# Performance work log

Hardware: AMD Instinct MI355X
Metric: run time of the kernel (lower is better)

Reference implementation:

```python
import jax, jax.numpy as jnp
import numpy as np

HEADS = 8
DIM_HEAD = 64
SCALE = DIM_HEAD ** (-0.5)


def setup_inputs() -> dict:
    key = jax.random.key(0)
    ks = jax.random.split(key, 6)
    x = jax.random.normal(ks[0], (4, 2048, 1024), dtype=jnp.float32)
    context = jax.random.normal(ks[1], (4, 512, 768), dtype=jnp.float32)
    # linear weights stored as (in, out); init scaled like nn.Linear default-ish
    Wq = jax.random.normal(ks[2], (1024, 512), dtype=jnp.float32) * (1.0 / np.sqrt(1024))
    Wk = jax.random.normal(ks[3], (768, 512), dtype=jnp.float32) * (1.0 / np.sqrt(768))
    Wv = jax.random.normal(ks[4], (768, 512), dtype=jnp.float32) * (1.0 / np.sqrt(768))
    Wo = jax.random.normal(ks[5], (512, 1024), dtype=jnp.float32) * (1.0 / np.sqrt(512))
    return {"x": x, "context": context, "Wq": Wq, "Wk": Wk, "Wv": Wv, "Wo": Wo}


def reference(x, context, Wq, Wk, Wv, Wo):
    # projections: [b, i, inner], [b, j, inner]
    q = jnp.einsum('bid,de->bie', x, Wq)
    k = jnp.einsum('bjd,de->bje', context, Wk)
    v = jnp.einsum('bjd,de->bje', context, Wv)
    b, i, _ = q.shape
    j = k.shape[1]
    # split heads: [b, h, seq, c]
    q = q.reshape(b, i, HEADS, DIM_HEAD).transpose(0, 2, 1, 3)
    k = k.reshape(b, j, HEADS, DIM_HEAD).transpose(0, 2, 1, 3)
    v = v.reshape(b, j, HEADS, DIM_HEAD).transpose(0, 2, 1, 3)
    scores = jnp.einsum('bhic,bhjc->bhij', q, k) * SCALE
    attn = jax.nn.softmax(scores, axis=-1)
    out = jnp.einsum('bhij,bhjc->bhic', attn, v)  # [b, h, i, c]
    out = out.transpose(0, 2, 1, 3).reshape(b, i, HEADS * DIM_HEAD)
    return jnp.einsum('bie,ed->bid', out, Wo)
```

## Files before the change

kernel.cpp:

```cpp
#include <hip/hip_runtime.h>
#include <stdint.h>

typedef unsigned short u16;
typedef __attribute__((ext_vector_type(8))) short short8;
typedef __attribute__((ext_vector_type(4))) float f32x4;

#define MFMA16(a, b, c) __builtin_amdgcn_mfma_f32_16x16x32_bf16((a), (b), (c), 0, 0, 0)

__device__ __forceinline__ u16 f2bf(float f) {
  unsigned int u = __float_as_uint(f);
  u += 0x7FFFu + ((u >> 16) & 1u);
  return (u16)(u >> 16);
}

__device__ __forceinline__ void gload16(const void* g, u16* lds) {
  __builtin_amdgcn_global_load_lds(
      (const __attribute__((address_space(1))) unsigned int*)g,
      (__attribute__((address_space(3))) unsigned int*)lds, 16, 0, 0);
}

__global__ void prep_all(const float* __restrict__ x, u16* __restrict__ xb, int n4x,
                         const float* __restrict__ cx, u16* __restrict__ cb, int n4c,
                         const float* __restrict__ Wq, const float* __restrict__ Wk,
                         const float* __restrict__ Wv, const float* __restrict__ Wo,
                         u16* __restrict__ wqT, u16* __restrict__ wkvT,
                         u16* __restrict__ woT) {
  __shared__ float tile[32][33];
  int z = blockIdx.z;
  int tx = threadIdx.x, ty = threadIdx.y;
  if (z == 4) {
    int bid = blockIdx.y * 32 + blockIdx.x;
    int tid = ty * 32 + tx;
    int idx = bid * 256 + tid, stride = 1024 * 256;
    int total = n4x + n4c;
    for (int i2 = idx; i2 < total; i2 += stride) {
      float4 v = (i2 < n4x) ? ((const float4*)x)[i2] : ((const float4*)cx)[i2 - n4x];
      ushort4 o;
      o.x = f2bf(v.x); o.y = f2bf(v.y); o.z = f2bf(v.z); o.w = f2bf(v.w);
      if (i2 < n4x) ((ushort4*)xb)[i2] = o; else ((ushort4*)cb)[i2 - n4x] = o;
    }
    return;
  }
  const float* src; u16* dst; int R, C; float scale = 1.0f;
  if (z == 0)      { src = Wq; dst = wqT;  R = 1024; C = 512;  scale = 0.125f; }
  else if (z == 1) { src = Wk; dst = wkvT; R = 768;  C = 512;  }
  else if (z == 2) { src = Wv; dst = wkvT + (size_t)512 * 768; R = 768; C = 512; }
  else             { src = Wo; dst = woT;  R = 512;  C = 1024; }
  int bx = blockIdx.x * 32, by = blockIdx.y * 32;
  if (bx >= C || by >= R) return;
#pragma unroll
  for (int i = 0; i < 4; ++i)
    tile[ty + 8 * i][tx] = src[(size_t)(by + ty + 8 * i) * C + bx + tx];
  __syncthreads();
#pragma unroll
  for (int i = 0; i < 4; ++i)
    dst[(size_t)(bx + ty + 8 * i) * R + by + tx] = f2bf(tile[tx][ty + 8 * i] * scale);
}

template <int MODE>
__device__ __forceinline__ void gemm_body(const u16* __restrict__ A,
                                          const u16* __restrict__ BT,
                                          void* __restrict__ C0p,
                                          void* __restrict__ C1p,
                                          int tm, int tn, int K, int N, u16* smem) {
  u16* As = smem;
  u16* Bs = smem + 8192;
  const int t = threadIdx.x;
  const int w = t >> 6, l = t & 63, lr = l & 15, lg = l >> 4;
  const int wr = w >> 1, wc = w & 1;

  f32x4 acc[4][2];
#pragma unroll
  for (int mi = 0; mi < 4; ++mi)
#pragma unroll
    for (int ni = 0; ni < 2; ++ni) acc[mi][ni] = (f32x4){0.f, 0.f, 0.f, 0.f};

  for (int kt = 0; kt < K; kt += 64) {
#pragma unroll
    for (int p = 0; p < 4; ++p) {
      int idx = p * 256 + t, row = idx >> 3, cg = idx & 7;
      gload16(A + (size_t)(tm + row) * K + kt + ((cg ^ (row & 7)) * 8),
              As + (p * 256 + (t & 192)) * 8);
    }
#pragma unroll
    for (int pb = 0; pb < 2; ++pb) {
      int idx = pb * 256 + t, row = idx >> 3, cg = idx & 7;
      gload16(BT + (size_t)(tn + row) * K + kt + ((cg ^ (row & 7)) * 8),
              Bs + (pb * 256 + (t & 192)) * 8);
    }
    __syncthreads();
    short8 af[4][2], bf[2][2];
#pragma unroll
    for (int mi = 0; mi < 4; ++mi)
#pragma unroll
      for (int kk = 0; kk < 2; ++kk)
        af[mi][kk] = *(const short8*)
            &As[(wr * 64 + mi * 16 + lr) * 64 + (((kk * 4 + lg) ^ (lr & 7)) * 8)];
#pragma unroll
    for (int ni = 0; ni < 2; ++ni)
#pragma unroll
      for (int kk = 0; kk < 2; ++kk)
        bf[ni][kk] = *(const short8*)
            &Bs[(wc * 32 + ni * 16 + lr) * 64 + (((kk * 4 + lg) ^ (lr & 7)) * 8)];
#pragma unroll
    for (int mi = 0; mi < 4; ++mi)
#pragma unroll
      for (int ni = 0; ni < 2; ++ni) {
        acc[mi][ni] = MFMA16(af[mi][0], bf[ni][0], acc[mi][ni]);
        acc[mi][ni] = MFMA16(af[mi][1], bf[ni][1], acc[mi][ni]);
      }
    __syncthreads();
  }

  if (MODE == 2 && tn >= 512) {
    u16* tile = smem;
#pragma unroll
    for (int mi = 0; mi < 4; ++mi)
#pragma unroll
      for (int ni = 0; ni < 2; ++ni) {
        ushort4 pk;
        pk.x = f2bf(acc[mi][ni][0]); pk.y = f2bf(acc[mi][ni][1]);
        pk.z = f2bf(acc[mi][ni][2]); pk.w = f2bf(acc[mi][ni][3]);
        *(ushort4*)&tile[(wc * 32 + ni * 16 + lr) * 136 + wr * 64 + mi * 16 + lg * 4] = pk;
      }
    __syncthreads();
    int bh = ((tm >> 9) << 3) + ((tn - 512) >> 6);
    u16* dst = (u16*)C1p + (size_t)bh * 64 * 512 + (tm & 511);
#pragma unroll
    for (int p = 0; p < 4; ++p) {
      int c = (p * 256 + t) >> 4, jj = (t & 15) * 8;
      short8 v = *(const short8*)&tile[c * 136 + jj];
      *(short8*)(dst + (size_t)c * 512 + jj) = v;
    }
    return;
  }

#pragma unroll
  for (int mi = 0; mi < 4; ++mi)
#pragma unroll
    for (int ni = 0; ni < 2; ++ni)
#pragma unroll
      for (int r = 0; r < 4; ++r) {
        int rg = tm + wr * 64 + mi * 16 + lg * 4 + r;
        int cg = tn + wc * 32 + ni * 16 + lr;
        float val = acc[mi][ni][r];
        if (MODE == 0) {
          ((float*)C0p)[(size_t)rg * N + cg] = val;
        } else if (MODE == 1) {
          ((u16*)C0p)[(((size_t)(rg >> 11) * 8 + (cg >> 6)) * 2048 + (rg & 2047)) * 64 +
                      (cg & 63)] = f2bf(val);
        } else {
          ((u16*)C0p)[(((size_t)(rg >> 9) * 8 + (cg >> 6)) * 512 + (rg & 511)) * 64 +
                      (cg & 63)] = f2bf(val);
        }
      }
}

__global__ __launch_bounds__(256) void gemm_qkv(const u16* __restrict__ xb,
                                                const u16* __restrict__ wqT,
                                                u16* __restrict__ qhb,
                                                const u16* __restrict__ cb,
                                                const u16* __restrict__ wkvT,
                                                u16* __restrict__ khb,
                                                u16* __restrict__ vtb) {
  __shared__ __align__(16) u16 smem[12288];
  int gid = (int)blockIdx.x;
  gid = (gid & 7) * 96 + (gid >> 3);
  if (gid < 512) {
    gemm_body<1>(xb, wqT, qhb, nullptr, (gid >> 3) * 128, (gid & 7) * 64, 1024, 512, smem);
  } else {
    int g2 = gid - 512;
    gemm_body<2>(cb, wkvT, khb, vtb, (g2 >> 4) * 128, (g2 & 15) * 64, 768, 1024, smem);
  }
}

__global__ __launch_bounds__(256) void gemm_o(const u16* __restrict__ aob,
                                              const u16* __restrict__ woT,
                                              float* __restrict__ out) {
  __shared__ __align__(16) u16 smem[12288];
  int gid = (int)blockIdx.x;
  gid = (gid & 7) * 128 + (gid >> 3);
  gemm_body<0>(aob, woT, out, nullptr, (gid >> 4) * 128, (gid & 15) * 64, 512, 1024, smem);
}

__global__ __launch_bounds__(512, 2) void attn_kernel(const u16* __restrict__ qhb,
                                                      const u16* __restrict__ khb,
                                                      const u16* __restrict__ vtb,
                                                      u16* __restrict__ aob) {
  __shared__ __align__(16) u16 kb[512 * 64];
  __shared__ __align__(16) u16 vb[64 * 512];
  __shared__ __align__(16) u16 pl[8][16 * 64];
  const int t = threadIdx.x, w = t >> 6, l = t & 63, i = l & 15, g = l >> 4;
  int lid = (int)blockIdx.x;
  lid = (lid & 7) * 64 + (lid >> 3);
  const int bh = lid >> 4, qh = lid & 15;
  const int i7 = i & 7;
  const int row0 = qh * 128 + w * 16;

  const u16* qp = qhb + ((size_t)bh * 2048 + row0) * 64;
  const u16* kp = khb + (size_t)bh * 512 * 64;
  const u16* vp = vtb + (size_t)bh * 64 * 512;

  short8 qa0 = *(const short8*)(qp + (size_t)i * 64 + g * 8);
  short8 qa1 = *(const short8*)(qp + (size_t)i * 64 + 32 + g * 8);

  const int wbase = (t & 448) * 8;

#pragma unroll
  for (int p = 0; p < 8; ++p) {
    int s = p * 512 + t;
    int r = s >> 3, cg = s & 7;
    gload16(kp + (size_t)r * 64 + ((cg ^ (r & 7)) * 8), kb + p * 4096 + wbase);
  }
#pragma unroll
  for (int p = 0; p < 8; ++p) {
    int s = p * 512 + t;
    int r = s >> 6, cg = s & 63;
    gload16(vp + (size_t)r * 512 + ((cg ^ (r & 7)) * 8), vb + p * 4096 + wbase);
  }
  __syncthreads();

  f32x4 sc[32];
#pragma unroll
  for (int jt = 0; jt < 32; ++jt) {
    int r = jt * 16 + i;
    short8 k0 = *(const short8*)&kb[r * 64 + ((g ^ i7) * 8)];
    short8 k1 = *(const short8*)&kb[r * 64 + (((4 + g) ^ i7) * 8)];
    f32x4 a = (f32x4){0.f, 0.f, 0.f, 0.f};
    a = MFMA16(k0, qa0, a);
    a = MFMA16(k1, qa1, a);
    sc[jt] = a;
  }

  f32x4 vm = sc[0];
#pragma unroll
  for (int jt = 1; jt < 32; ++jt) {
#pragma unroll
    for (int r = 0; r < 4; ++r) vm[r] = fmaxf(vm[r], sc[jt][r]);
  }
  float mx = fmaxf(fmaxf(vm[0], vm[1]), fmaxf(vm[2], vm[3]));
  mx = fmaxf(mx, __shfl_xor(mx, 16));
  mx = fmaxf(mx, __shfl_xor(mx, 32));
  float sum = 0.f;
#pragma unroll
  for (int jt = 0; jt < 32; ++jt) {
#pragma unroll
    for (int r = 0; r < 4; ++r) {
      float e = __expf(sc[jt][r] - mx);
      sc[jt][r] = e;
      sum += e;
    }
  }
  sum += __shfl_xor(sum, 16);
  sum += __shfl_xor(sum, 32);
  float inv = 1.f / sum;

  u16* pw = pl[w];
  f32x4 oac[4];
#pragma unroll
  for (int ct = 0; ct < 4; ++ct) oac[ct] = (f32x4){0.f, 0.f, 0.f, 0.f};

#pragma unroll
  for (int c8 = 0; c8 < 8; ++c8) {
#pragma unroll
    for (int tt = 0; tt < 4; ++tt) {
      int jt = c8 * 4 + tt;
      unsigned w0, w1;
      asm("v_cvt_pk_bf16_f32 %0, %1, %2" : "=v"(w0) : "v"(sc[jt][0]), "v"(sc[jt][1]));
      asm("v_cvt_pk_bf16_f32 %0, %1, %2" : "=v"(w1) : "v"(sc[jt][2]), "v"(sc[jt][3]));
      uint2 pk2; pk2.x = w0; pk2.y = w1;
      *(uint2*)&pw[i * 64 + ((tt * 16 + g * 4) ^ (i7 * 8))] = pk2;
    }
    asm volatile("s_waitcnt lgkmcnt(0)" ::: "memory");
    __builtin_amdgcn_sched_barrier(0);
#pragma unroll
    for (int T2 = 0; T2 < 2; ++T2) {
      short8 pa = *(const short8*)&pw[i * 64 + ((T2 * 32 + g * 8) ^ (i7 * 8))];
      int jg = c8 * 8 + T2 * 4 + g;
#pragma unroll
      for (int ct = 0; ct < 4; ++ct) {
        int vr = ct * 16 + i;
        short8 vf = *(const short8*)&vb[vr * 512 + ((jg ^ (vr & 7)) * 8)];
        oac[ct] = MFMA16(pa, vf, oac[ct]);
      }
    }
    asm volatile("" ::: "memory");
  }

  float iv[4];
#pragma unroll
  for (int r = 0; r < 4; ++r) iv[r] = __shfl(inv, (l & 48) + g * 4 + r);
  u16* op = aob + ((size_t)(bh >> 3) * 2048 + row0) * 512 + (bh & 7) * 64;
#pragma unroll
  for (int ct = 0; ct < 4; ++ct)
#pragma unroll
    for (int r = 0; r < 4; ++r)
      op[(size_t)(g * 4 + r) * 512 + ct * 16 + i] = f2bf(oac[ct][r] * iv[r]);
}

extern "C" void kernel_launch(void* const* d_in, const int* in_sizes, int n_in,
                              void* d_out, int out_size, void* d_ws, size_t ws_size,
                              hipStream_t stream) {
  const float* x  = (const float*)d_in[0];
  const float* cx = (const float*)d_in[1];
  const float* Wq = (const float*)d_in[2];
  const float* Wk = (const float*)d_in[3];
  const float* Wv = (const float*)d_in[4];
  const float* Wo = (const float*)d_in[5];
  float* out = (float*)d_out;

  char* p = (char*)d_ws;
  u16* xb   = (u16*)p; p += (size_t)8388608 * 2;
  u16* cb   = (u16*)p; p += (size_t)1572864 * 2;
  u16* wqT  = (u16*)p; p += (size_t)524288 * 2;
  u16* wkvT = (u16*)p; p += (size_t)786432 * 2;
  u16* woT  = (u16*)p; p += (size_t)524288 * 2;
  u16* qhb  = (u16*)p; p += (size_t)4194304 * 2;
  u16* khb  = (u16*)p; p += (size_t)1048576 * 2;
  u16* vtb  = (u16*)p; p += (size_t)1048576 * 2;
  u16* aob  = (u16*)p; p += (size_t)4194304 * 2;

  prep_all<<<dim3(32, 32, 5), dim3(32, 8), 0, stream>>>(
      x, xb, 8388608 / 4, cx, cb, 1572864 / 4, Wq, Wk, Wv, Wo, wqT, wkvT, woT);
  gemm_qkv<<<768, 256, 0, stream>>>(xb, wqT, qhb, cb, wkvT, khb, vtb);
  attn_kernel<<<512, 512, 0, stream>>>(qhb, khb, vtb, aob);
  gemm_o<<<1024, 256, 0, stream>>>(aob, woT, out);
}
```

Baseline: 67.59 us.

## Double-buffer LDS tiles in GEMM kernels to overlap global loads with MFMA

Splits the GEMM shared-memory staging into two buffers. The next K-tile is issued with global_load_lds while MFMAs run on the current tile, which hides global-load latency behind compute. LDS per block doubles to 48 KB, which may reduce occupancy. Only one barrier per iteration remains, and ordering depends on the loads of the next stage completing by the barrier at the end of the iteration.

```diff
diff --git a/kernel.cpp b/kernel.cpp
--- a/kernel.cpp
+++ b/kernel.cpp
@@ -63,32 +63,41 @@
                                           void* __restrict__ C0p,
                                           void* __restrict__ C1p,
                                           int tm, int tn, int K, int N, u16* smem) {
-  u16* As = smem;
-  u16* Bs = smem + 8192;
   const int t = threadIdx.x;
   const int w = t >> 6, l = t & 63, lr = l & 15, lg = l >> 4;
   const int wr = w >> 1, wc = w & 1;
 
+#define QSTAGE(buf, kt)                                                        \
+  {                                                                            \
+    u16* As_ = smem + (buf) * 12288;                                           \
+    u16* Bs_ = As_ + 8192;                                                     \
+    _Pragma("unroll") for (int p = 0; p < 4; ++p) {                            \
+      int idx = p * 256 + t, row = idx >> 3, cg = idx & 7;                     \
+      gload16(A + (size_t)(tm + row) * K + (kt) + ((cg ^ (row & 7)) * 8),      \
+              As_ + (p * 256 + (t & 192)) * 8);                                \
+    }                                                                          \
+    _Pragma("unroll") for (int pb = 0; pb < 2; ++pb) {                         \
+      int idx = pb * 256 + t, row = idx >> 3, cg = idx & 7;                    \
+      gload16(BT + (size_t)(tn + row) * K + (kt) + ((cg ^ (row & 7)) * 8),     \
+              Bs_ + (pb * 256 + (t & 192)) * 8);                               \
+    }                                                                          \
+  }
+
   f32x4 acc[4][2];
 #pragma unroll
   for (int mi = 0; mi < 4; ++mi)
 #pragma unroll
     for (int ni = 0; ni < 2; ++ni) acc[mi][ni] = (f32x4){0.f, 0.f, 0.f, 0.f};
 
-  for (int kt = 0; kt < K; kt += 64) {
-#pragma unroll
-    for (int p = 0; p < 4; ++p) {
-      int idx = p * 256 + t, row = idx >> 3, cg = idx & 7;
-      gload16(A + (size_t)(tm + row) * K + kt + ((cg ^ (row & 7)) * 8),
-              As + (p * 256 + (t & 192)) * 8);
-    }
-#pragma unroll
-    for (int pb = 0; pb < 2; ++pb) {
-      int idx = pb * 256 + t, row = idx >> 3, cg = idx & 7;
-      gload16(BT + (size_t)(tn + row) * K + kt + ((cg ^ (row & 7)) * 8),
-              Bs + (pb * 256 + (t & 192)) * 8);
-    }
-    __syncthreads();
+  const int nt = K >> 6;
+  QSTAGE(0, 0);
+  __syncthreads();
+
+  for (int ti = 0; ti < nt; ++ti) {
+    int buf = ti & 1;
+    if (ti + 1 < nt) QSTAGE(buf ^ 1, (ti + 1) * 64);
+    const u16* As = smem + buf * 12288;
+    const u16* Bs = As + 8192;
     short8 af[4][2], bf[2][2];
 #pragma unroll
     for (int mi = 0; mi < 4; ++mi)
@@ -111,6 +120,7 @@
       }
     __syncthreads();
   }
+#undef QSTAGE
 
   if (MODE == 2 && tn >= 512) {
     u16* tile = smem;
@@ -163,7 +173,7 @@
                                                 const u16* __restrict__ wkvT,
                                                 u16* __restrict__ khb,
                                                 u16* __restrict__ vtb) {
-  __shared__ __align__(16) u16 smem[12288];
+  __shared__ __align__(16) u16 smem[24576];
   int gid = (int)blockIdx.x;
   gid = (gid & 7) * 96 + (gid >> 3);
   if (gid < 512) {
@@ -177,7 +187,7 @@
 __global__ __launch_bounds__(256) void gemm_o(const u16* __restrict__ aob,
                                               const u16* __restrict__ woT,
                                               float* __restrict__ out) {
-  __shared__ __align__(16) u16 smem[12288];
+  __shared__ __align__(16) u16 smem[24576];
   int gid = (int)blockIdx.x;
   gid = (gid & 7) * 128 + (gid >> 3);
   gemm_body<0>(aob, woT, out, nullptr, (gid >> 4) * 128, (gid & 15) * 64, 512, 1024, smem);
```

Result: no change. 68.71 us (+1.6%).
